# Optimization experiments

Hardware: AMD Instinct MI355X
Metric: run time of the kernel (lower is better)

Reference implementation:

```python
import jax, jax.numpy as jnp
import numpy as np

ROUTE = 64            # route_size (square)
NLEV = 4              # resolution_num = [0,1,2,3]
LOSS_W = (1.0, 1.0, 1.0, 1.0)


def _sumpool(x, k):
    # non-overlapping sum pool, kernel=stride=k; x: (B,1,H,W) with H,W divisible by k
    B, C, H, W = x.shape
    return x.reshape(B, C, H // k, k, W // k, k).sum(axis=(3, 5))


def _up_nearest(x, k):
    # nearest upsample by integer factor k on the two trailing dims
    return jnp.repeat(jnp.repeat(x, k, axis=2), k, axis=3)


def _unfold(x, k):
    # F.unfold(x, k, stride=k) then .transpose(2,1).view(B,L,k,k) for C==1
    B, C, H, W = x.shape
    ph, pw = H // k, W // k
    return x.reshape(B, ph, k, pw, k).transpose(0, 1, 3, 2, 4).reshape(B, ph * pw, k, k)


def _fold(p, H, W, k):
    # inverse of _unfold: p (B, L, k, k) -> (B,1,H,W)
    B, L, _, _ = p.shape
    ph, pw = H // k, W // k
    return p.reshape(B, ph, pw, k, k).transpose(0, 1, 3, 2, 4).reshape(B, 1, H, W)


def setup_inputs() -> dict:
    key = jax.random.key(0)
    ks = jax.random.split(key, 8)
    B, H = 8, 1024
    d = {}
    for i in range(NLEV):
        s = (B, 1, H >> i, H >> i)
        d[f'out{i}'] = jax.random.uniform(ks[i], s, dtype=jnp.float32)
        d[f'gt{i}'] = jax.random.uniform(ks[4 + i], s, dtype=jnp.float32)
    return d


def reference(out0, out1, out2, out3, gt0, gt1, gt2, gt3):
    out_list = [out0, out1, out2, out3]
    label_list = [gt0, gt1, gt2, gt3]
    B, _, H, W = out0.shape

    # ---- get_moe_label: per-patch routing score on detached maps ----
    scores = []
    for i in range(NLEV):
        k = ROUTE >> i
        pre = jax.lax.stop_gradient(out_list[i])
        gt = jax.lax.stop_gradient(label_list[i])
        err = (pre - gt) ** 2
        patch_err = _sumpool(err, k)                      # (B,1,ph,pw)
        patch_mse = patch_err / (k * k)
        fractions = _sumpool(gt, k)
        scores.append(patch_mse + patch_err / (fractions + 1e-10))
    score = jnp.concatenate(scores, axis=1)               # (B,4,ph,pw)
    moe_label = jnp.argmin(score, axis=1, keepdims=True)  # (B,1,ph,pw) int

    # mask_gt = scatter one-hot of moe_label along channel dim
    mask_gt = (moe_label == jnp.arange(NLEV, dtype=moe_label.dtype)[None, :, None, None]).astype(score.dtype)

    mask_add = jnp.ones_like(mask_gt[:, :1])              # (B,1,ph,pw)
    loss = jnp.zeros((), dtype=out0.dtype)
    label_patch = None
    moe_flat = moe_label.reshape(B, -1)                   # (B, L)

    for i in range(NLEV):
        k = ROUTE >> i
        loss_mask = _up_nearest(mask_add, k)              # matches out_list[i] spatial size
        hard = jnp.mean((out_list[i] * loss_mask - label_list[i] * loss_mask) ** 2)
        loss = loss + hard * LOSS_W[i]
        if i == 0:
            lp = label_list[0] * _up_nearest(mask_gt[:, 0:1], ROUTE)
            label_patch = _unfold(lp, ROUTE)              # (B, L, 64, 64)
        else:
            gsl = _unfold(label_list[i], k)               # (B, L, k, k)
            pad = (ROUTE - k) // 2
            gsl = jnp.pad(gsl, ((0, 0), (0, 0), (pad, pad), (pad, pad)), constant_values=0.2)
            pick = (moe_flat == i)[:, :, None, None]
            label_patch = label_patch + gsl * pick
        mask_add = mask_add - mask_gt[:, i:i + 1]

    label_patch = _fold(label_patch, H, W, ROUTE)         # (B,1,H,W)
    return loss[None], label_patch, moe_label, score
```

## Files before the change

kernel.cpp:

```cpp
#include <hip/hip_runtime.h>


#define NPATCH 2048

__global__ __launch_bounds__(256) void fused_kernel(
    const float* __restrict__ out0, const float* __restrict__ gt0,
    const float* __restrict__ out1, const float* __restrict__ gt1,
    const float* __restrict__ out2, const float* __restrict__ gt2,
    const float* __restrict__ out3, const float* __restrict__ gt3,
    float* __restrict__ scoreOut,
    float* __restrict__ moeF,
    float* __restrict__ lab,
    double* __restrict__ lossTerm)
{
    const int q = blockIdx.x;
    const int px = q >> 7;
    const int row = q & 127;
    const int b = row >> 4;
    const int py = row & 15;
    const int l = (py << 4) | px;
    const int p = (b << 8) | l;

    const float* PO[4] = {out0, out1, out2, out3};
    const float* PG[4] = {gt0, gt1, gt2, gt3};

    float err[4], gts[4];

    #pragma unroll
    for (int lev = 0; lev < 4; ++lev) {
        const int k  = 64 >> lev;
        const int W  = 1024 >> lev;
        const int kv = k >> 2;
        const int nvec = k * kv;
        const int rowBase = py * k, colBase = px * k;
        const size_t base = (size_t)b * W * W;
        const float* po = PO[lev];
        const float* pg = PG[lev];

        float e = 0.f, g = 0.f;
        for (int idx = threadIdx.x; idx < nvec; idx += 256) {
            int r = idx / kv;
            int c = (idx % kv) * 4;
            size_t off = base + (size_t)(rowBase + r) * W + (colBase + c);
            float4 o = *(const float4*)(po + off);
            float4 qv = *(const float4*)(pg + off);
            float dx = o.x - qv.x, dy = o.y - qv.y, dz = o.z - qv.z, dw = o.w - qv.w;
            e += dx * dx + dy * dy + dz * dz + dw * dw;
            g += qv.x + qv.y + qv.z + qv.w;
        }
        err[lev] = e; gts[lev] = g;
    }

    for (int s = 32; s; s >>= 1) {
        #pragma unroll
        for (int i = 0; i < 4; ++i) {
            err[i] += __shfl_down(err[i], s, 64);
            gts[i] += __shfl_down(gts[i], s, 64);
        }
    }
    __shared__ float se[4][4], sg[4][4];
    __shared__ int smv;
    const int wave = threadIdx.x >> 6, lane = threadIdx.x & 63;
    if (lane == 0) {
        #pragma unroll
        for (int i = 0; i < 4; ++i) { se[i][wave] = err[i]; sg[i][wave] = gts[i]; }
    }
    __syncthreads();
    if (threadIdx.x == 0) {
        float E[4], S[4];
        #pragma unroll
        for (int i = 0; i < 4; ++i) {
            E[i] = se[i][0] + se[i][1] + se[i][2] + se[i][3];
            float G = sg[i][0] + sg[i][1] + sg[i][2] + sg[i][3];
            float kk = (float)((64 >> i) * (64 >> i));
            S[i] = E[i] / kk + E[i] / (G + 1e-10f);
            scoreOut[b * 1024 + i * 256 + l] = S[i];
        }
        int m = 0; float best = S[0];
        #pragma unroll
        for (int i = 1; i < 4; ++i)
            if (S[i] < best) { best = S[i]; m = i; }
        moeF[p] = (float)m;
        smv = m;
        double t = (double)E[0] / 8388608.0;
        if (m >= 1) t += (double)E[1] / 2097152.0;
        if (m >= 2) t += (double)E[2] / 524288.0;
        if (m >= 3) t += (double)E[3] / 131072.0;
        lossTerm[p] = t;
    }
    __syncthreads();
    const int m = smv;

    const size_t labBase = (size_t)b * 1048576 + (size_t)(py << 6) * 1024 + (px << 6);

    if (m == 0) {
        for (int idx = threadIdx.x; idx < 1024; idx += 256) {
            int y = idx >> 4, j = idx & 15;
            size_t R0 = labBase + (size_t)y * 1024;
            if (j < 15) {
                int x = 3 + 4 * j;
                float4 v;
                v.x = gt0[R0 + x];
                v.y = gt0[R0 + x + 1];
                v.z = gt0[R0 + x + 2];
                v.w = gt0[R0 + x + 3];
                *(float4*)(lab + R0 + x) = v;
            } else {
                lab[R0]      = gt0[R0];
                lab[R0 + 1]  = gt0[R0 + 1];
                lab[R0 + 2]  = gt0[R0 + 2];
                lab[R0 + 63] = gt0[R0 + 63];
            }
        }
    } else {
        const int k = 64 >> m, pad = (64 - k) >> 1, W = 1024 >> m;
        const float* gt = (m == 1) ? gt1 : (m == 2) ? gt2 : gt3;
        const size_t gbase = (size_t)b * W * W + (size_t)(py * k) * W + px * k;
        for (int idx = threadIdx.x; idx < 1024; idx += 256) {
            int y = idx >> 4, j = idx & 15;
            size_t R0 = labBase + (size_t)y * 1024;
            int iy = y - pad;
            bool rowIn = (unsigned)iy < (unsigned)k;
            const float* grow = gt + gbase + (size_t)iy * W;
            if (j < 15) {
                int x = 3 + 4 * j;
                float4 v;
                #pragma unroll
                for (int u = 0; u < 4; ++u) {
                    int ix = x + u - pad;
                    float vv = 0.2f;
                    if (rowIn && (unsigned)ix < (unsigned)k) vv = grow[ix];
                    ((float*)&v)[u] = vv;
                }
                *(float4*)(lab + R0 + x) = v;
            } else {
                #pragma unroll
                for (int u = 0; u < 3; ++u) {
                    int ix = u - pad;
                    float vv = 0.2f;
                    if (rowIn && (unsigned)ix < (unsigned)k) vv = grow[ix];
                    lab[R0 + u] = vv;
                }
                int ix = 63 - pad;
                float vv = 0.2f;
                if (rowIn && (unsigned)ix < (unsigned)k) vv = grow[ix];
                lab[R0 + 63] = vv;
            }
        }
    }
}

__global__ __launch_bounds__(256) void loss_kernel(
    const double* __restrict__ lossTerm, float* __restrict__ lossOut)
{
    double t = 0.0;
    for (int i = threadIdx.x; i < NPATCH; i += 256) t += lossTerm[i];
    for (int s = 32; s; s >>= 1) t += __shfl_down(t, s, 64);
    __shared__ double sd[4];
    const int wave = threadIdx.x >> 6, lane = threadIdx.x & 63;
    if (lane == 0) sd[wave] = t;
    __syncthreads();
    if (threadIdx.x == 0)
        lossOut[0] = (float)(sd[0] + sd[1] + sd[2] + sd[3]);
}

extern "C" void kernel_launch(void* const* d_in, const int* in_sizes, int n_in,
                              void* d_out, int out_size, void* d_ws, size_t ws_size,
                              hipStream_t stream) {
    const float* out0 = (const float*)d_in[0];
    const float* gt0  = (const float*)d_in[1];
    const float* out1 = (const float*)d_in[2];
    const float* gt1  = (const float*)d_in[3];
    const float* out2 = (const float*)d_in[4];
    const float* gt2  = (const float*)d_in[5];
    const float* out3 = (const float*)d_in[6];
    const float* gt3  = (const float*)d_in[7];

    float* o = (float*)d_out;
    float* lossOut  = o;
    float* labOut   = o + 1;
    float* moeFOut  = o + 8388609;
    float* scoreOut = o + 8390657;

    double* lossTerm = (double*)d_ws;

    fused_kernel<<<NPATCH, 256, 0, stream>>>(
        out0, gt0, out1, gt1, out2, gt2, out3, gt3,
        scoreOut, moeFOut, labOut, lossTerm);
    loss_kernel<<<1, 256, 0, stream>>>(lossTerm, lossOut);
}
```

Baseline: 30.65 us.

## Map one wavefront per patch and drop block-level shared-memory reductions

Each patch is now handled by a single 64-lane wavefront, with two patches per 128-thread block, instead of one 256-thread block per patch. Per-level loops are specialised with constant trip counts and unrolled. The reduction uses xor shuffles so every lane gets the totals, which removes the shared-memory stage and both __syncthreads. The cost is fewer threads per patch and more serial loads per lane, so each wave has more memory latency to hide.

```diff
diff --git a/kernel.cpp b/kernel.cpp
--- a/kernel.cpp
+++ b/kernel.cpp
@@ -3,7 +3,7 @@
 
 #define NPATCH 2048
 
-__global__ __launch_bounds__(256) void fused_kernel(
+__global__ __launch_bounds__(128) void fused_kernel(
     const float* __restrict__ out0, const float* __restrict__ gt0,
     const float* __restrict__ out1, const float* __restrict__ gt1,
     const float* __restrict__ out2, const float* __restrict__ gt2,
@@ -13,88 +13,113 @@
     float* __restrict__ lab,
     double* __restrict__ lossTerm)
 {
-    const int q = blockIdx.x;
-    const int px = q >> 7;
-    const int row = q & 127;
+    const int w = threadIdx.x >> 6;
+    const int lane = threadIdx.x & 63;
+    const int pp = (blockIdx.x << 1) | w;
+    const int px = pp >> 7;
+    const int row = pp & 127;
     const int b = row >> 4;
     const int py = row & 15;
     const int l = (py << 4) | px;
     const int p = (b << 8) | l;
 
-    const float* PO[4] = {out0, out1, out2, out3};
-    const float* PG[4] = {gt0, gt1, gt2, gt3};
-
-    float err[4], gts[4];
+    float e0 = 0.f, g0 = 0.f, e1 = 0.f, g1 = 0.f;
+    float e2 = 0.f, g2 = 0.f, e3 = 0.f, g3 = 0.f;
+
+    {
+        const size_t base = (size_t)b * 1048576;
+        const int rb = py << 6, cb = px << 6;
+        #pragma unroll 4
+        for (int it = 0; it < 16; ++it) {
+            int idx = (it << 6) | lane;
+            int r = idx >> 4, c = (idx & 15) << 2;
+            size_t off = base + (size_t)(rb + r) * 1024 + (cb + c);
+            float4 o = *(const float4*)(out0 + off);
+            float4 q = *(const float4*)(gt0 + off);
+            float dx = o.x - q.x, dy = o.y - q.y, dz = o.z - q.z, dw = o.w - q.w;
+            e0 += dx * dx + dy * dy + dz * dz + dw * dw;
+            g0 += q.x + q.y + q.z + q.w;
+        }
+    }
+    {
+        const size_t base = (size_t)b * 262144;
+        const int rb = py << 5, cb = px << 5;
+        #pragma unroll
+        for (int it = 0; it < 4; ++it) {
+            int idx = (it << 6) | lane;
+            int r = idx >> 3, c = (idx & 7) << 2;
+            size_t off = base + (size_t)(rb + r) * 512 + (cb + c);
+            float4 o = *(const float4*)(out1 + off);
+            float4 q = *(const float4*)(gt1 + off);
+            float dx = o.x - q.x, dy = o.y - q.y, dz = o.z - q.z, dw = o.w - q.w;
+            e1 += dx * dx + dy * dy + dz * dz + dw * dw;
+            g1 += q.x + q.y + q.z + q.w;
+        }
+    }
+    {
+        const size_t base = (size_t)b * 65536;
+        int r = lane >> 2, c = (lane & 3) << 2;
+        size_t off = base + (size_t)((py << 4) + r) * 256 + ((px << 4) + c);
+        float4 o = *(const float4*)(out2 + off);
+        float4 q = *(const float4*)(gt2 + off);
+        float dx = o.x - q.x, dy = o.y - q.y, dz = o.z - q.z, dw = o.w - q.w;
+        e2 = dx * dx + dy * dy + dz * dz + dw * dw;
+        g2 = q.x + q.y + q.z + q.w;
+    }
+    {
+        const size_t base = (size_t)b * 16384;
+        int tt = lane & 15;
+        int r = tt >> 1, c = (tt & 1) << 2;
+        size_t off = base + (size_t)((py << 3) + r) * 128 + ((px << 3) + c);
+        float4 o = *(const float4*)(out3 + off);
+        float4 q = *(const float4*)(gt3 + off);
+        float dx = o.x - q.x, dy = o.y - q.y, dz = o.z - q.z, dw = o.w - q.w;
+        float e = dx * dx + dy * dy + dz * dz + dw * dw;
+        float g = q.x + q.y + q.z + q.w;
+        bool act = (lane < 16);
+        e3 = act ? e : 0.f;
+        g3 = act ? g : 0.f;
+    }
 
     #pragma unroll
-    for (int lev = 0; lev < 4; ++lev) {
-        const int k  = 64 >> lev;
-        const int W  = 1024 >> lev;
-        const int kv = k >> 2;
-        const int nvec = k * kv;
-        const int rowBase = py * k, colBase = px * k;
-        const size_t base = (size_t)b * W * W;
-        const float* po = PO[lev];
-        const float* pg = PG[lev];
-
-        float e = 0.f, g = 0.f;
-        for (int idx = threadIdx.x; idx < nvec; idx += 256) {
-            int r = idx / kv;
-            int c = (idx % kv) * 4;
-            size_t off = base + (size_t)(rowBase + r) * W + (colBase + c);
-            float4 o = *(const float4*)(po + off);
-            float4 qv = *(const float4*)(pg + off);
-            float dx = o.x - qv.x, dy = o.y - qv.y, dz = o.z - qv.z, dw = o.w - qv.w;
-            e += dx * dx + dy * dy + dz * dz + dw * dw;
-            g += qv.x + qv.y + qv.z + qv.w;
-        }
-        err[lev] = e; gts[lev] = g;
-    }
-
-    for (int s = 32; s; s >>= 1) {
-        #pragma unroll
-        for (int i = 0; i < 4; ++i) {
-            err[i] += __shfl_down(err[i], s, 64);
-            gts[i] += __shfl_down(gts[i], s, 64);
-        }
-    }
-    __shared__ float se[4][4], sg[4][4];
-    __shared__ int smv;
-    const int wave = threadIdx.x >> 6, lane = threadIdx.x & 63;
+    for (int s = 1; s < 64; s <<= 1) {
+        e0 += __shfl_xor(e0, s, 64);  g0 += __shfl_xor(g0, s, 64);
+        e1 += __shfl_xor(e1, s, 64);  g1 += __shfl_xor(g1, s, 64);
+        e2 += __shfl_xor(e2, s, 64);  g2 += __shfl_xor(g2, s, 64);
+        e3 += __shfl_xor(e3, s, 64);  g3 += __shfl_xor(g3, s, 64);
+    }
+
+    float E[4] = {e0, e1, e2, e3};
+    float G[4] = {g0, g1, g2, g3};
+    float S[4];
+    #pragma unroll
+    for (int i = 0; i < 4; ++i) {
+        float kk = (float)((64 >> i) * (64 >> i));
+        S[i] = E[i] / kk + E[i] / (G[i] + 1e-10f);
+    }
+    int m = 0; float best = S[0];
+    #pragma unroll
+    for (int i = 1; i < 4; ++i)
+        if (S[i] < best) { best = S[i]; m = i; }
+
     if (lane == 0) {
         #pragma unroll
-        for (int i = 0; i < 4; ++i) { se[i][wave] = err[i]; sg[i][wave] = gts[i]; }
-    }
-    __syncthreads();
-    if (threadIdx.x == 0) {
-        float E[4], S[4];
-        #pragma unroll
-        for (int i = 0; i < 4; ++i) {
-            E[i] = se[i][0] + se[i][1] + se[i][2] + se[i][3];
-            float G = sg[i][0] + sg[i][1] + sg[i][2] + sg[i][3];
-            float kk = (float)((64 >> i) * (64 >> i));
-            S[i] = E[i] / kk + E[i] / (G + 1e-10f);
+        for (int i = 0; i < 4; ++i)
             scoreOut[b * 1024 + i * 256 + l] = S[i];
-        }
-        int m = 0; float best = S[0];
-        #pragma unroll
-        for (int i = 1; i < 4; ++i)
-            if (S[i] < best) { best = S[i]; m = i; }
         moeF[p] = (float)m;
-        smv = m;
-        double t = (double)E[0] / 8388608.0;
-        if (m >= 1) t += (double)E[1] / 2097152.0;
-        if (m >= 2) t += (double)E[2] / 524288.0;
-        if (m >= 3) t += (double)E[3] / 131072.0;
+        double t = (double)e0 / 8388608.0;
+        if (m >= 1) t += (double)e1 / 2097152.0;
+        if (m >= 2) t += (double)e2 / 524288.0;
+        if (m >= 3) t += (double)e3 / 131072.0;
         lossTerm[p] = t;
     }
-    __syncthreads();
-    const int m = smv;
 
     const size_t labBase = (size_t)b * 1048576 + (size_t)(py << 6) * 1024 + (px << 6);
 
     if (m == 0) {
-        for (int idx = threadIdx.x; idx < 1024; idx += 256) {
+        #pragma unroll 4
+        for (int it = 0; it < 16; ++it) {
+            int idx = (it << 6) | lane;
             int y = idx >> 4, j = idx & 15;
             size_t R0 = labBase + (size_t)y * 1024;
             if (j < 15) {
@@ -116,7 +141,9 @@
         const int k = 64 >> m, pad = (64 - k) >> 1, W = 1024 >> m;
         const float* gt = (m == 1) ? gt1 : (m == 2) ? gt2 : gt3;
         const size_t gbase = (size_t)b * W * W + (size_t)(py * k) * W + px * k;
-        for (int idx = threadIdx.x; idx < 1024; idx += 256) {
+        #pragma unroll 4
+        for (int it = 0; it < 16; ++it) {
+            int idx = (it << 6) | lane;
             int y = idx >> 4, j = idx & 15;
             size_t R0 = labBase + (size_t)y * 1024;
             int iy = y - pad;
@@ -184,7 +211,7 @@
 
     double* lossTerm = (double*)d_ws;
 
-    fused_kernel<<<NPATCH, 256, 0, stream>>>(
+    fused_kernel<<<NPATCH / 2, 128, 0, stream>>>(
         out0, gt0, out1, gt1, out2, gt2, out3, gt3,
         scoreOut, moeFOut, labOut, lossTerm);
     loss_kernel<<<1, 256, 0, stream>>>(lossTerm, lossOut);
```

New measurement: 32.57 us. 6.3% more time.

## Keep gt values in registers and stage label patch through shared memory

Applied to the files above, without the earlier changes.

The score pass now unrolls each level with a fixed thread mapping and keeps the loaded gt float4 values in registers. After routing, the selected level's values plus the 0.2 padding are written into a 64x64 shared-memory tile, which is then streamed to the misaligned label output. This removes the second global read of gt, which previously used scalar, unaligned loads. The cost is extra registers for the held values, 16KB of shared memory per block, and one more barrier, which may lower occupancy.

```diff
diff --git a/kernel.cpp b/kernel.cpp
--- a/kernel.cpp
+++ b/kernel.cpp
@@ -13,6 +13,10 @@
     float* __restrict__ lab,
     double* __restrict__ lossTerm)
 {
+    __shared__ float tile[64][64];
+    __shared__ float se[4][4], sg[4][4];
+    __shared__ int smv;
+
     const int q = blockIdx.x;
     const int px = q >> 7;
     const int row = q & 127;
@@ -20,35 +24,61 @@
     const int py = row & 15;
     const int l = (py << 4) | px;
     const int p = (b << 8) | l;
-
-    const float* PO[4] = {out0, out1, out2, out3};
-    const float* PG[4] = {gt0, gt1, gt2, gt3};
-
-    float err[4], gts[4];
-
-    #pragma unroll
-    for (int lev = 0; lev < 4; ++lev) {
-        const int k  = 64 >> lev;
-        const int W  = 1024 >> lev;
-        const int kv = k >> 2;
-        const int nvec = k * kv;
-        const int rowBase = py * k, colBase = px * k;
-        const size_t base = (size_t)b * W * W;
-        const float* po = PO[lev];
-        const float* pg = PG[lev];
-
+    const int t = threadIdx.x;
+
+    float err[4] = {0.f, 0.f, 0.f, 0.f}, gts[4] = {0.f, 0.f, 0.f, 0.f};
+
+    float4 q0[4];
+    {
+        const size_t base = (size_t)b * 1048576;
+        const int rb = py << 6, cb = px << 6;
         float e = 0.f, g = 0.f;
-        for (int idx = threadIdx.x; idx < nvec; idx += 256) {
-            int r = idx / kv;
-            int c = (idx % kv) * 4;
-            size_t off = base + (size_t)(rowBase + r) * W + (colBase + c);
-            float4 o = *(const float4*)(po + off);
-            float4 qv = *(const float4*)(pg + off);
+        #pragma unroll
+        for (int it = 0; it < 4; ++it) {
+            int idx = t + (it << 8);
+            int r = idx >> 4, c = (idx & 15) << 2;
+            size_t off = base + (size_t)(rb + r) * 1024 + (cb + c);
+            float4 o = *(const float4*)(out0 + off);
+            float4 qv = *(const float4*)(gt0 + off);
+            q0[it] = qv;
             float dx = o.x - qv.x, dy = o.y - qv.y, dz = o.z - qv.z, dw = o.w - qv.w;
             e += dx * dx + dy * dy + dz * dz + dw * dw;
             g += qv.x + qv.y + qv.z + qv.w;
         }
-        err[lev] = e; gts[lev] = g;
+        err[0] = e; gts[0] = g;
+    }
+    float4 q1;
+    {
+        const size_t base = (size_t)b * 262144;
+        int r = t >> 3, c = (t & 7) << 2;
+        size_t off = base + (size_t)((py << 5) + r) * 512 + ((px << 5) + c);
+        float4 o = *(const float4*)(out1 + off);
+        q1 = *(const float4*)(gt1 + off);
+        float dx = o.x - q1.x, dy = o.y - q1.y, dz = o.z - q1.z, dw = o.w - q1.w;
+        err[1] = dx * dx + dy * dy + dz * dz + dw * dw;
+        gts[1] = q1.x + q1.y + q1.z + q1.w;
+    }
+    float4 q2 = {0.f, 0.f, 0.f, 0.f};
+    if (t < 64) {
+        const size_t base = (size_t)b * 65536;
+        int r = t >> 2, c = (t & 3) << 2;
+        size_t off = base + (size_t)((py << 4) + r) * 256 + ((px << 4) + c);
+        float4 o = *(const float4*)(out2 + off);
+        q2 = *(const float4*)(gt2 + off);
+        float dx = o.x - q2.x, dy = o.y - q2.y, dz = o.z - q2.z, dw = o.w - q2.w;
+        err[2] = dx * dx + dy * dy + dz * dz + dw * dw;
+        gts[2] = q2.x + q2.y + q2.z + q2.w;
+    }
+    float4 q3 = {0.f, 0.f, 0.f, 0.f};
+    if (t < 16) {
+        const size_t base = (size_t)b * 16384;
+        int r = t >> 1, c = (t & 1) << 2;
+        size_t off = base + (size_t)((py << 3) + r) * 128 + ((px << 3) + c);
+        float4 o = *(const float4*)(out3 + off);
+        q3 = *(const float4*)(gt3 + off);
+        float dx = o.x - q3.x, dy = o.y - q3.y, dz = o.z - q3.z, dw = o.w - q3.w;
+        err[3] = dx * dx + dy * dy + dz * dz + dw * dw;
+        gts[3] = q3.x + q3.y + q3.z + q3.w;
     }
 
     for (int s = 32; s; s >>= 1) {
@@ -58,15 +88,13 @@
             gts[i] += __shfl_down(gts[i], s, 64);
         }
     }
-    __shared__ float se[4][4], sg[4][4];
-    __shared__ int smv;
-    const int wave = threadIdx.x >> 6, lane = threadIdx.x & 63;
+    const int wave = t >> 6, lane = t & 63;
     if (lane == 0) {
         #pragma unroll
         for (int i = 0; i < 4; ++i) { se[i][wave] = err[i]; sg[i][wave] = gts[i]; }
     }
     __syncthreads();
-    if (threadIdx.x == 0) {
+    if (t == 0) {
         float E[4], S[4];
         #pragma unroll
         for (int i = 0; i < 4; ++i) {
@@ -82,70 +110,75 @@
             if (S[i] < best) { best = S[i]; m = i; }
         moeF[p] = (float)m;
         smv = m;
-        double t = (double)E[0] / 8388608.0;
-        if (m >= 1) t += (double)E[1] / 2097152.0;
-        if (m >= 2) t += (double)E[2] / 524288.0;
-        if (m >= 3) t += (double)E[3] / 131072.0;
-        lossTerm[p] = t;
+        double tt = (double)E[0] / 8388608.0;
+        if (m >= 1) tt += (double)E[1] / 2097152.0;
+        if (m >= 2) tt += (double)E[2] / 524288.0;
+        if (m >= 3) tt += (double)E[3] / 131072.0;
+        lossTerm[p] = tt;
     }
     __syncthreads();
     const int m = smv;
 
+    const float4 pv = {0.2f, 0.2f, 0.2f, 0.2f};
+    if (m == 0) {
+        #pragma unroll
+        for (int it = 0; it < 4; ++it) {
+            int idx = t + (it << 8);
+            int r = idx >> 4, c = (idx & 15) << 2;
+            *(float4*)&tile[r][c] = q0[it];
+        }
+    } else if (m == 1) {
+        { int r = t >> 3, c = (t & 7) << 2; *(float4*)&tile[16 + r][16 + c] = q1; }
+        #pragma unroll
+        for (int z = 0; z < 3; ++z) {
+            int idx = t + (z << 8);
+            int prow, pcol;
+            if (idx < 256)      { prow = idx >> 4;                pcol = (idx & 15) << 2; }
+            else if (idx < 512) { int w = idx - 256; prow = 48 + (w >> 4); pcol = (w & 15) << 2; }
+            else                { int w = idx - 512; prow = 16 + (w >> 3);
+                                  int s = w & 7; pcol = (s < 4) ? (s << 2) : (48 + ((s - 4) << 2)); }
+            *(float4*)&tile[prow][pcol] = pv;
+        }
+    } else if (m == 2) {
+        if (t < 64) { int r = t >> 2, c = (t & 3) << 2; *(float4*)&tile[24 + r][24 + c] = q2; }
+        for (int idx = t; idx < 960; idx += 256) {
+            int prow, pcol;
+            if (idx < 384)      { prow = idx >> 4;                pcol = (idx & 15) << 2; }
+            else if (idx < 768) { int w = idx - 384; prow = 40 + (w >> 4); pcol = (w & 15) << 2; }
+            else                { int w = idx - 768; prow = 24 + w / 12;
+                                  int s = w % 12; pcol = (s < 6) ? (s << 2) : (40 + ((s - 6) << 2)); }
+            *(float4*)&tile[prow][pcol] = pv;
+        }
+    } else {
+        if (t < 16) { int r = t >> 1, c = (t & 1) << 2; *(float4*)&tile[28 + r][28 + c] = q3; }
+        for (int idx = t; idx < 1008; idx += 256) {
+            int prow, pcol;
+            if (idx < 448)      { prow = idx >> 4;                pcol = (idx & 15) << 2; }
+            else if (idx < 896) { int w = idx - 448; prow = 36 + (w >> 4); pcol = (w & 15) << 2; }
+            else                { int w = idx - 896; prow = 28 + w / 14;
+                                  int s = w % 14; pcol = (s < 7) ? (s << 2) : (36 + ((s - 7) << 2)); }
+            *(float4*)&tile[prow][pcol] = pv;
+        }
+    }
+    __syncthreads();
+
     const size_t labBase = (size_t)b * 1048576 + (size_t)(py << 6) * 1024 + (px << 6);
-
-    if (m == 0) {
-        for (int idx = threadIdx.x; idx < 1024; idx += 256) {
-            int y = idx >> 4, j = idx & 15;
-            size_t R0 = labBase + (size_t)y * 1024;
-            if (j < 15) {
-                int x = 3 + 4 * j;
-                float4 v;
-                v.x = gt0[R0 + x];
-                v.y = gt0[R0 + x + 1];
-                v.z = gt0[R0 + x + 2];
-                v.w = gt0[R0 + x + 3];
-                *(float4*)(lab + R0 + x) = v;
-            } else {
-                lab[R0]      = gt0[R0];
-                lab[R0 + 1]  = gt0[R0 + 1];
-                lab[R0 + 2]  = gt0[R0 + 2];
-                lab[R0 + 63] = gt0[R0 + 63];
-            }
-        }
-    } else {
-        const int k = 64 >> m, pad = (64 - k) >> 1, W = 1024 >> m;
-        const float* gt = (m == 1) ? gt1 : (m == 2) ? gt2 : gt3;
-        const size_t gbase = (size_t)b * W * W + (size_t)(py * k) * W + px * k;
-        for (int idx = threadIdx.x; idx < 1024; idx += 256) {
-            int y = idx >> 4, j = idx & 15;
-            size_t R0 = labBase + (size_t)y * 1024;
-            int iy = y - pad;
-            bool rowIn = (unsigned)iy < (unsigned)k;
-            const float* grow = gt + gbase + (size_t)iy * W;
-            if (j < 15) {
-                int x = 3 + 4 * j;
-                float4 v;
-                #pragma unroll
-                for (int u = 0; u < 4; ++u) {
-                    int ix = x + u - pad;
-                    float vv = 0.2f;
-                    if (rowIn && (unsigned)ix < (unsigned)k) vv = grow[ix];
-                    ((float*)&v)[u] = vv;
-                }
-                *(float4*)(lab + R0 + x) = v;
-            } else {
-                #pragma unroll
-                for (int u = 0; u < 3; ++u) {
-                    int ix = u - pad;
-                    float vv = 0.2f;
-                    if (rowIn && (unsigned)ix < (unsigned)k) vv = grow[ix];
-                    lab[R0 + u] = vv;
-                }
-                int ix = 63 - pad;
-                float vv = 0.2f;
-                if (rowIn && (unsigned)ix < (unsigned)k) vv = grow[ix];
-                lab[R0 + 63] = vv;
-            }
+    for (int idx = t; idx < 1024; idx += 256) {
+        int y = idx >> 4, j = idx & 15;
+        size_t R0 = labBase + (size_t)y * 1024;
+        if (j < 15) {
+            int x = 3 + 4 * j;
+            float4 v;
+            v.x = tile[y][x];
+            v.y = tile[y][x + 1];
+            v.z = tile[y][x + 2];
+            v.w = tile[y][x + 3];
+            *(float4*)(lab + R0 + x) = v;
+        } else {
+            lab[R0]      = tile[y][0];
+            lab[R0 + 1]  = tile[y][1];
+            lab[R0 + 2]  = tile[y][2];
+            lab[R0 + 63] = tile[y][63];
         }
     }
 }
```

After: 30.92 us. About the same (+0.9%).
